# Performance work log

Measured on AMD Instinct MI355X. Metric: run time of the kernel, lower is better.

The kernel has to match this reference:

```python
import jax, jax.numpy as jnp
import numpy as np

# DAG configuration (fixed, mirrors the networkx dG used at construction time)
B = 4096          # batch
N_INP = 4096      # genes
L0 = 512          # leaf GO terms, each mapped to G disjoint genes
G = 8             # genes per leaf term
H = 16            # module_neurons (uniform per-module hidden size)
FAN = 8           # children per internal module -> input size FAN*H = 128
L1, L2 = 64, 8    # internal level sizes; root has L2=8 children


def setup_inputs() -> dict:
    key = jax.random.key(0)
    ks = jax.random.split(key, 8)
    s = lambda *sh: 0.1
    x = jax.random.normal(ks[0], (B, N_INP), dtype=jnp.float32)
    # Gene (RestrictedLayer) effective weights: kernel*connections is one-hot,
    # so only kernel[gene_idx[m,j], j] survives -> store as [L0, G] + bias.
    Wg = jax.random.normal(ks[1], (L0, G), dtype=jnp.float32) * 0.1
    bg = jax.random.normal(ks[2], (L0, G), dtype=jnp.float32) * 0.1
    # Per-level module Dense kernels (sigmoid, no bias)
    W0 = jax.random.normal(ks[3], (L0, G, H), dtype=jnp.float32) * 0.1       # leaf terms: G -> H
    W1 = jax.random.normal(ks[4], (L1, FAN * H, H), dtype=jnp.float32) * 0.1  # 128 -> 16
    W2 = jax.random.normal(ks[5], (L2, FAN * H, H), dtype=jnp.float32) * 0.1  # 128 -> 16
    W3 = jax.random.normal(ks[6], (FAN * H, H), dtype=jnp.float32) * 0.1      # root: 128 -> 16
    Wf = jax.random.normal(ks[7], (H, 1), dtype=jnp.float32) * 0.1            # final linear, no bias
    return {"x": x, "Wg": Wg, "bg": bg, "W0": W0, "W1": W1, "W2": W2,
            "W3": W3, "Wf": Wf}


def reference(x, Wg, bg, W0, W1, W2, W3, Wf):
    b = x.shape[0]
    # Input gene layers (RestrictedLayer, linear activation):
    # leaf m owns contiguous genes [m*G, (m+1)*G) -> gather is a reshape.
    gene_out = x.reshape(b, L0, G) * Wg + bg                    # [B, L0, G]
    # Level 0 (leaf GO terms): Dense(G->H), sigmoid, no bias
    h0 = jax.nn.sigmoid(jnp.einsum('bmg,mgh->bmh', gene_out, W0))   # [B, L0, H]
    # Level 1: concat FAN children's H outputs -> Dense(FAN*H -> H), sigmoid
    h1 = jax.nn.sigmoid(jnp.einsum('bmk,mkh->bmh',
                                   h0.reshape(b, L1, FAN * H), W1))  # [B, L1, H]
    # Level 2
    h2 = jax.nn.sigmoid(jnp.einsum('bmk,mkh->bmh',
                                   h1.reshape(b, L2, FAN * H), W2))  # [B, L2, H]
    # Root 'GO:output'
    hr = jax.nn.sigmoid(h2.reshape(b, FAN * H) @ W3)                 # [B, H]
    # Final Dense(1), linear, no bias
    return hr @ Wf                                                   # [B, 1]
```

## Files before the change

kernel.cpp:

```cpp
#include <hip/hip_runtime.h>
#include <hip/hip_bf16.h>


#define TB 16
#define XSS 520
#define H0S 1032
#define H1S 136

typedef __attribute__((ext_vector_type(8))) short short8;
typedef __attribute__((ext_vector_type(4))) float floatx4;

__device__ __forceinline__ float sigf(float v) {
    return __builtin_amdgcn_rcpf(1.0f + __expf(-v));
}
__device__ __forceinline__ float bflo(unsigned int p) {
    return __builtin_bit_cast(float, p << 16);
}
__device__ __forceinline__ float bfhi(unsigned int p) {
    return __builtin_bit_cast(float, p & 0xffff0000u);
}
__device__ __forceinline__ unsigned int f2bf_u32(float f) {
    unsigned int u = __builtin_bit_cast(unsigned int, f);
    return (u + 0x7fffu + ((u >> 16) & 1u)) >> 16;
}
__device__ __forceinline__ unsigned short f2bf(float f) {
    return (unsigned short)f2bf_u32(f);
}
__device__ __forceinline__ unsigned int f2bf2(float lo, float hi) {
    return f2bf_u32(lo) | (f2bf_u32(hi) << 16);
}

__global__ __launch_bounds__(256) void k_prep(
    const float* __restrict__ W1, const float* __restrict__ W2,
    unsigned short* __restrict__ W1t, unsigned short* __restrict__ W2t)
{
    __shared__ float wl[128 * 17];
    const int mb = blockIdx.x;
    const float* src = (mb < 64) ? (W1 + (size_t)mb * 2048)
                                 : (W2 + (size_t)(mb - 64) * 2048);
    unsigned short* dst = (mb < 64) ? (W1t + (size_t)mb * 2048)
                                    : (W2t + (size_t)(mb - 64) * 2048);
    const int tid = threadIdx.x;
#pragma unroll
    for (int i = 0; i < 8; ++i) {
        const int idx = tid + i * 256;
        wl[(idx >> 4) * 17 + (idx & 15)] = src[idx];
    }
    __syncthreads();
#pragma unroll
    for (int i = 0; i < 4; ++i) {
        const int u  = tid + i * 256;
        const int h  = u >> 6;
        const int k  = (u & 63) * 2;
        ((unsigned int*)dst)[u] = f2bf2(wl[k * 17 + h], wl[(k + 1) * 17 + h]);
    }
}

__global__ __launch_bounds__(256) void k_tree(
    const float* __restrict__ x, const float* __restrict__ Wg,
    const float* __restrict__ bg, const float* __restrict__ W0,
    const unsigned short* __restrict__ W1t, const unsigned short* __restrict__ W2t,
    float* __restrict__ h2ws)
{
    __shared__ __align__(16) unsigned short xs[TB * XSS];
    __shared__ __align__(16) unsigned short h0s[TB * H0S];
    unsigned short* h1u = xs;

    const int tid  = threadIdx.x;
    const int s    = blockIdx.x & 7;
    const int b0   = (blockIdx.x >> 3) * TB;
    const int lane = tid & 63;
    const int wv   = tid >> 6;

    const float* xbase = x + (size_t)b0 * 4096 + s * 512;
    uint2 xp[8];
#pragma unroll
    for (int t = 0; t < 8; ++t) {
        const int i = tid + t * 256;
        const int r = i >> 7, c4 = i & 127;
        const float4 v = *(const float4*)(xbase + (size_t)r * 4096 + c4 * 4);
        xp[t] = make_uint2(f2bf2(v.x, v.y), f2bf2(v.z, v.w));
    }

    const int m_l = tid >> 2;
    const int hq  = tid & 3;
    const int m   = s * 64 + m_l;
    float4 w0r[8];
#pragma unroll
    for (int g = 0; g < 8; ++g)
        w0r[g] = *(const float4*)(W0 + (size_t)m * 128 + g * 16 + hq * 4);
    const float4 wg0 = *(const float4*)(Wg + m * 8);
    const float4 wg1 = *(const float4*)(Wg + m * 8 + 4);
    const float4 bg0 = *(const float4*)(bg + m * 8);
    const float4 bg1 = *(const float4*)(bg + m * 8 + 4);

    const int n = lane & 15, q = lane >> 4;
    short8 w1r[2][4];
#pragma unroll
    for (int jj = 0; jj < 2; ++jj) {
        const unsigned short* w1m =
            W1t + ((size_t)(s * 8 + wv * 2 + jj) * 16 + n) * 128 + q * 8;
#pragma unroll
        for (int ks = 0; ks < 4; ++ks)
            w1r[jj][ks] = *(const short8*)(w1m + ks * 32);
    }
    short8 w2r[4];
    if (wv == 0) {
        const unsigned short* w2m = W2t + ((size_t)s * 16 + n) * 128 + q * 8;
#pragma unroll
        for (int ks = 0; ks < 4; ++ks) w2r[ks] = *(const short8*)(w2m + ks * 32);
    }

#pragma unroll
    for (int t = 0; t < 8; ++t) {
        const int i = tid + t * 256;
        const int r = i >> 7, c4 = i & 127;
        *(uint2*)&xs[r * XSS + c4 * 4] = xp[t];
    }
    __syncthreads();

    {
        unsigned short* h0base = &h0s[m_l * 16 + hq * 4];
#pragma unroll 4
        for (int b = 0; b < TB; ++b) {
            const uint4 xv = *(const uint4*)&xs[b * XSS + m_l * 8];
            float gene[8];
            gene[0] = fmaf(bflo(xv.x), wg0.x, bg0.x);
            gene[1] = fmaf(bfhi(xv.x), wg0.y, bg0.y);
            gene[2] = fmaf(bflo(xv.y), wg0.z, bg0.z);
            gene[3] = fmaf(bfhi(xv.y), wg0.w, bg0.w);
            gene[4] = fmaf(bflo(xv.z), wg1.x, bg1.x);
            gene[5] = fmaf(bfhi(xv.z), wg1.y, bg1.y);
            gene[6] = fmaf(bflo(xv.w), wg1.z, bg1.z);
            gene[7] = fmaf(bfhi(xv.w), wg1.w, bg1.w);
            float a0 = 0.f, a1 = 0.f, a2 = 0.f, a3 = 0.f;
#pragma unroll
            for (int g = 0; g < 8; ++g) {
                a0 = fmaf(gene[g], w0r[g].x, a0);
                a1 = fmaf(gene[g], w0r[g].y, a1);
                a2 = fmaf(gene[g], w0r[g].z, a2);
                a3 = fmaf(gene[g], w0r[g].w, a3);
            }
            *(uint2*)(h0base + b * H0S) =
                make_uint2(f2bf2(sigf(a0), sigf(a1)), f2bf2(sigf(a2), sigf(a3)));
        }
    }
    __syncthreads();

    {
#pragma unroll
        for (int jj = 0; jj < 2; ++jj) {
            const int j = wv * 2 + jj;
            const unsigned short* am = &h0s[n * H0S + j * 128 + q * 8];
            floatx4 acc = {0.f, 0.f, 0.f, 0.f};
#pragma unroll
            for (int ks = 0; ks < 4; ++ks) {
                const short8 av = *(const short8*)(am + ks * 32);
                acc = __builtin_amdgcn_mfma_f32_16x16x32_bf16(av, w1r[jj][ks], acc, 0, 0, 0);
            }
#pragma unroll
            for (int r = 0; r < 4; ++r)
                h1u[(q * 4 + r) * H1S + j * 16 + n] = f2bf(sigf(acc[r]));
        }
    }
    __syncthreads();

    if (wv == 0) {
        const unsigned short* am = &h1u[n * H1S + q * 8];
        floatx4 acc = {0.f, 0.f, 0.f, 0.f};
#pragma unroll
        for (int ks = 0; ks < 4; ++ks) {
            const short8 av = *(const short8*)(am + ks * 32);
            acc = __builtin_amdgcn_mfma_f32_16x16x32_bf16(av, w2r[ks], acc, 0, 0, 0);
        }
#pragma unroll
        for (int r = 0; r < 4; ++r)
            h2ws[(size_t)(b0 + q * 4 + r) * 128 + s * 16 + n] = sigf(acc[r]);
    }
}

__global__ __launch_bounds__(128) void k_root(
    const float* __restrict__ h2ws, const float* __restrict__ W3,
    const float* __restrict__ Wf, float* __restrict__ out)
{
    __shared__ float w3s[2048];
    __shared__ float wfs[16];
    const int tid = threadIdx.x;
#pragma unroll
    for (int t = 0; t < 16; ++t) w3s[tid + t * 128] = W3[tid + t * 128];
    if (tid < 16) wfs[tid] = Wf[tid];
    __syncthreads();

    const int h = tid & 15;
    const int b = blockIdx.x * 8 + (tid >> 4);
    const float4* hp = (const float4*)(h2ws + (size_t)b * 128);
    float acc = 0.f;
#pragma unroll
    for (int k4 = 0; k4 < 32; ++k4) {
        const float4 hv = hp[k4];
        acc = fmaf(hv.x, w3s[(k4 * 4 + 0) * 16 + h], acc);
        acc = fmaf(hv.y, w3s[(k4 * 4 + 1) * 16 + h], acc);
        acc = fmaf(hv.z, w3s[(k4 * 4 + 2) * 16 + h], acc);
        acc = fmaf(hv.w, w3s[(k4 * 4 + 3) * 16 + h], acc);
    }
    float v = sigf(acc) * wfs[h];
    v += __shfl_down(v, 8, 16);
    v += __shfl_down(v, 4, 16);
    v += __shfl_down(v, 2, 16);
    v += __shfl_down(v, 1, 16);
    if (h == 0) out[b] = v;
}

extern "C" void kernel_launch(void* const* d_in, const int* in_sizes, int n_in,
                              void* d_out, int out_size, void* d_ws, size_t ws_size,
                              hipStream_t stream) {
    const float* x  = (const float*)d_in[0];
    const float* Wg = (const float*)d_in[1];
    const float* bg = (const float*)d_in[2];
    const float* W0 = (const float*)d_in[3];
    const float* W1 = (const float*)d_in[4];
    const float* W2 = (const float*)d_in[5];
    const float* W3 = (const float*)d_in[6];
    const float* Wf = (const float*)d_in[7];
    float* out = (float*)d_out;

    float* h2 = (float*)d_ws;
    unsigned short* W1t = (unsigned short*)((char*)d_ws + (size_t)2 * 1024 * 1024);
    unsigned short* W2t = W1t + (size_t)64 * 2048;

    k_prep<<<dim3(72), dim3(256), 0, stream>>>(W1, W2, W1t, W2t);
    k_tree<<<dim3((4096 / TB) * 8), dim3(256), 0, stream>>>(x, Wg, bg, W0, W1t, W2t, h2);
    k_root<<<dim3(4096 / 8), dim3(128), 0, stream>>>(h2, W3, Wf, out);
}
```

Baseline: 120.3 us.

## Halve batch tile, read x directly from global, drop LDS staging

Reduces the per-block batch tile from 16 to 8 rows, doubling the number of blocks. The x shared-memory staging buffer and its bf16 round trip are removed, so x is read as float4 straight from global inside the leaf loop. W1/W2 fragments are now loaded inside the MFMA loops instead of being preloaded into registers. The MFMA rows are duplicated (n&7) and only half the outputs are stored. This trades MFMA utilisation and weight-load reuse for higher occupancy and less LDS traffic.

```diff
diff --git a/kernel.cpp b/kernel.cpp
--- a/kernel.cpp
+++ b/kernel.cpp
@@ -2,8 +2,7 @@
 #include <hip/hip_bf16.h>
 
 
-#define TB 16
-#define XSS 520
+#define TB 8
 #define H0S 1032
 #define H1S 136
 
@@ -12,12 +11,6 @@
 
 __device__ __forceinline__ float sigf(float v) {
     return __builtin_amdgcn_rcpf(1.0f + __expf(-v));
-}
-__device__ __forceinline__ float bflo(unsigned int p) {
-    return __builtin_bit_cast(float, p << 16);
-}
-__device__ __forceinline__ float bfhi(unsigned int p) {
-    return __builtin_bit_cast(float, p & 0xffff0000u);
 }
 __device__ __forceinline__ unsigned int f2bf_u32(float f) {
     unsigned int u = __builtin_bit_cast(unsigned int, f);
@@ -62,29 +55,18 @@
     const unsigned short* __restrict__ W1t, const unsigned short* __restrict__ W2t,
     float* __restrict__ h2ws)
 {
-    __shared__ __align__(16) unsigned short xs[TB * XSS];
     __shared__ __align__(16) unsigned short h0s[TB * H0S];
-    unsigned short* h1u = xs;
+    __shared__ __align__(16) unsigned short h1s[TB * H1S];
 
     const int tid  = threadIdx.x;
     const int s    = blockIdx.x & 7;
     const int b0   = (blockIdx.x >> 3) * TB;
     const int lane = tid & 63;
     const int wv   = tid >> 6;
-
-    const float* xbase = x + (size_t)b0 * 4096 + s * 512;
-    uint2 xp[8];
-#pragma unroll
-    for (int t = 0; t < 8; ++t) {
-        const int i = tid + t * 256;
-        const int r = i >> 7, c4 = i & 127;
-        const float4 v = *(const float4*)(xbase + (size_t)r * 4096 + c4 * 4);
-        xp[t] = make_uint2(f2bf2(v.x, v.y), f2bf2(v.z, v.w));
-    }
-
-    const int m_l = tid >> 2;
-    const int hq  = tid & 3;
-    const int m   = s * 64 + m_l;
+    const int m_l  = tid >> 2;
+    const int hq   = tid & 3;
+    const int m    = s * 64 + m_l;
+
     float4 w0r[8];
 #pragma unroll
     for (int g = 0; g < 8; ++g)
@@ -94,45 +76,22 @@
     const float4 bg0 = *(const float4*)(bg + m * 8);
     const float4 bg1 = *(const float4*)(bg + m * 8 + 4);
 
-    const int n = lane & 15, q = lane >> 4;
-    short8 w1r[2][4];
-#pragma unroll
-    for (int jj = 0; jj < 2; ++jj) {
-        const unsigned short* w1m =
-            W1t + ((size_t)(s * 8 + wv * 2 + jj) * 16 + n) * 128 + q * 8;
-#pragma unroll
-        for (int ks = 0; ks < 4; ++ks)
-            w1r[jj][ks] = *(const short8*)(w1m + ks * 32);
-    }
-    short8 w2r[4];
-    if (wv == 0) {
-        const unsigned short* w2m = W2t + ((size_t)s * 16 + n) * 128 + q * 8;
-#pragma unroll
-        for (int ks = 0; ks < 4; ++ks) w2r[ks] = *(const short8*)(w2m + ks * 32);
-    }
-
-#pragma unroll
-    for (int t = 0; t < 8; ++t) {
-        const int i = tid + t * 256;
-        const int r = i >> 7, c4 = i & 127;
-        *(uint2*)&xs[r * XSS + c4 * 4] = xp[t];
-    }
-    __syncthreads();
-
     {
+        const float* xb = x + (size_t)b0 * 4096 + s * 512 + m_l * 8;
         unsigned short* h0base = &h0s[m_l * 16 + hq * 4];
-#pragma unroll 4
+#pragma unroll
         for (int b = 0; b < TB; ++b) {
-            const uint4 xv = *(const uint4*)&xs[b * XSS + m_l * 8];
+            const float4 xv0 = *(const float4*)(xb + (size_t)b * 4096);
+            const float4 xv1 = *(const float4*)(xb + (size_t)b * 4096 + 4);
             float gene[8];
-            gene[0] = fmaf(bflo(xv.x), wg0.x, bg0.x);
-            gene[1] = fmaf(bfhi(xv.x), wg0.y, bg0.y);
-            gene[2] = fmaf(bflo(xv.y), wg0.z, bg0.z);
-            gene[3] = fmaf(bfhi(xv.y), wg0.w, bg0.w);
-            gene[4] = fmaf(bflo(xv.z), wg1.x, bg1.x);
-            gene[5] = fmaf(bfhi(xv.z), wg1.y, bg1.y);
-            gene[6] = fmaf(bflo(xv.w), wg1.z, bg1.z);
-            gene[7] = fmaf(bfhi(xv.w), wg1.w, bg1.w);
+            gene[0] = fmaf(xv0.x, wg0.x, bg0.x);
+            gene[1] = fmaf(xv0.y, wg0.y, bg0.y);
+            gene[2] = fmaf(xv0.z, wg0.z, bg0.z);
+            gene[3] = fmaf(xv0.w, wg0.w, bg0.w);
+            gene[4] = fmaf(xv1.x, wg1.x, bg1.x);
+            gene[5] = fmaf(xv1.y, wg1.y, bg1.y);
+            gene[6] = fmaf(xv1.z, wg1.z, bg1.z);
+            gene[7] = fmaf(xv1.w, wg1.w, bg1.w);
             float a0 = 0.f, a1 = 0.f, a2 = 0.f, a3 = 0.f;
 #pragma unroll
             for (int g = 0; g < 8; ++g) {
@@ -147,35 +106,45 @@
     }
     __syncthreads();
 
+    const int n = lane & 15, q = lane >> 4;
     {
 #pragma unroll
         for (int jj = 0; jj < 2; ++jj) {
             const int j = wv * 2 + jj;
-            const unsigned short* am = &h0s[n * H0S + j * 128 + q * 8];
+            const unsigned short* w1m =
+                W1t + ((size_t)(s * 8 + j) * 16 + n) * 128 + q * 8;
+            const unsigned short* am = &h0s[(n & 7) * H0S + j * 128 + q * 8];
             floatx4 acc = {0.f, 0.f, 0.f, 0.f};
 #pragma unroll
             for (int ks = 0; ks < 4; ++ks) {
                 const short8 av = *(const short8*)(am + ks * 32);
-                acc = __builtin_amdgcn_mfma_f32_16x16x32_bf16(av, w1r[jj][ks], acc, 0, 0, 0);
+                const short8 bv = *(const short8*)(w1m + ks * 32);
+                acc = __builtin_amdgcn_mfma_f32_16x16x32_bf16(av, bv, acc, 0, 0, 0);
             }
-#pragma unroll
-            for (int r = 0; r < 4; ++r)
-                h1u[(q * 4 + r) * H1S + j * 16 + n] = f2bf(sigf(acc[r]));
+            if (q < 2) {
+#pragma unroll
+                for (int r = 0; r < 4; ++r)
+                    h1s[(q * 4 + r) * H1S + j * 16 + n] = f2bf(sigf(acc[r]));
+            }
         }
     }
     __syncthreads();
 
     if (wv == 0) {
-        const unsigned short* am = &h1u[n * H1S + q * 8];
+        const unsigned short* w2m = W2t + ((size_t)s * 16 + n) * 128 + q * 8;
+        const unsigned short* am = &h1s[(n & 7) * H1S + q * 8];
         floatx4 acc = {0.f, 0.f, 0.f, 0.f};
 #pragma unroll
         for (int ks = 0; ks < 4; ++ks) {
             const short8 av = *(const short8*)(am + ks * 32);
-            acc = __builtin_amdgcn_mfma_f32_16x16x32_bf16(av, w2r[ks], acc, 0, 0, 0);
-        }
-#pragma unroll
-        for (int r = 0; r < 4; ++r)
-            h2ws[(size_t)(b0 + q * 4 + r) * 128 + s * 16 + n] = sigf(acc[r]);
+            const short8 bv = *(const short8*)(w2m + ks * 32);
+            acc = __builtin_amdgcn_mfma_f32_16x16x32_bf16(av, bv, acc, 0, 0, 0);
+        }
+        if (q < 2) {
+#pragma unroll
+            for (int r = 0; r < 4; ++r)
+                h2ws[(size_t)(b0 + q * 4 + r) * 128 + s * 16 + n] = sigf(acc[r]);
+        }
     }
 }
 
```

Measured after the change: 129.9 us. +8.1%, slower.
